# Optimization experiments

Hardware: AMD Instinct MI355X
Metric: run time of the kernel (lower is better)

The kernel has to match this reference:

```python
import jax, jax.numpy as jnp
import numpy as np

B, D, H, E, K = 4096, 1024, 4096, 8, 2

def setup_inputs() -> dict:
    key = jax.random.key(0)
    ks = jax.random.split(key, 6)
    return {
        "x_modality": jax.random.normal(ks[0], (B, D), dtype=jnp.float32),
        "expert_indices": jax.random.randint(ks[1], (B, K), 0, E, dtype=jnp.int32),
        "hard_weights": jax.random.uniform(ks[2], (B, K), dtype=jnp.float32),
        "w1": jax.random.normal(ks[3], (E, D, H), dtype=jnp.float32) * (1.0 / np.sqrt(D)),
        "b1": jnp.zeros((E, H), dtype=jnp.float32),
        "w2": jax.random.normal(ks[4], (E, H, D), dtype=jnp.float32) * (1.0 / np.sqrt(H)),
        "b2": jnp.zeros((E, D), dtype=jnp.float32),
    }

def reference(x_modality, expert_indices, hard_weights, w1, b1, w2, b2):
    b = x_modality.shape[0]
    # Per-token gate per expert: sum of hard_weights over top_k slots routed to that expert.
    gates = jnp.zeros((b, E), dtype=x_modality.dtype)
    gates = gates.at[jnp.arange(b)[:, None], expert_indices].add(hard_weights)  # [b, E]
    # Dense expert compute (small fixed E), then gated combine.
    h = jax.nn.gelu(jnp.einsum("bd,edh->ebh", x_modality, w1) + b1[:, None, :], approximate=False)
    y = jnp.einsum("ebh,ehd->ebd", h, w2) + b2[:, None, :]  # [E, b, D]
    return jnp.einsum("be,ebd->bd", gates, y)
```

## Files before the change

kernel.cpp:

```cpp
#include <hip/hip_runtime.h>
#include <hip/hip_bf16.h>
#include <math.h>

#define NB 4096
#define ND 1024
#define NH 4096
#define NE 8
#define NKK 2
#define NROWS (NB*NKK)
#define MAXT 72

typedef __attribute__((ext_vector_type(8))) short short8;
typedef __attribute__((ext_vector_type(4))) float f32x4;

__device__ __forceinline__ void gload_lds16(const void* g, void* l) {
    __builtin_amdgcn_global_load_lds(
        (const __attribute__((address_space(1))) unsigned int*)g,
        (__attribute__((address_space(3))) unsigned int*)l, 16, 0, 0);
}

__device__ __forceinline__ unsigned short f2bf(float f) {
    __hip_bfloat16 h = __float2bfloat16(f);
    return *reinterpret_cast<unsigned short*>(&h);
}

__device__ __forceinline__ float fast_gelu(float x) {
    float xs  = x * 0.70710678118654752f;
    float axs = fabsf(xs);
    float t   = __builtin_amdgcn_rcpf(1.0f + 0.3275911f * axs);
    float p   = t * (0.254829592f + t * (-0.284496736f + t * (1.421413741f +
                t * (-1.453152027f + t * 1.061405429f))));
    float e   = __expf(-xs * xs);
    float erf_abs = 1.0f - p * e;
    float erf = copysignf(erf_abs, x);
    return 0.5f * x * (1.0f + erf);
}


__global__ void k_cvt_x(const float* __restrict__ in, __hip_bfloat16* __restrict__ out, int n8) {
    int i = blockIdx.x * 256 + threadIdx.x;
    if (i >= n8) return;
    const float4* p = reinterpret_cast<const float4*>(in) + (size_t)i * 2;
    float4 a = p[0], b = p[1];
    ushort4 lo, hi;
    lo.x = f2bf(a.x); lo.y = f2bf(a.y); lo.z = f2bf(a.z); lo.w = f2bf(a.w);
    hi.x = f2bf(b.x); hi.y = f2bf(b.y); hi.z = f2bf(b.z); hi.w = f2bf(b.w);
    reinterpret_cast<ushort4*>(out)[(size_t)i*2]   = lo;
    reinterpret_cast<ushort4*>(out)[(size_t)i*2+1] = hi;
}

__global__ void k_transpose_cvt(const float* __restrict__ in, __hip_bfloat16* __restrict__ out,
                                int R, int C) {
    __shared__ float tile[64][68];
    const size_t ebase = (size_t)blockIdx.z * R * C;
    const int r0 = blockIdx.y * 64, c0 = blockIdx.x * 64;
    const int t = threadIdx.x;
    const int lr = t >> 4, lc4 = (t & 15) * 4;
    #pragma unroll
    for (int i = 0; i < 4; ++i) {
        int r = lr + i * 16;
        float4 v = *reinterpret_cast<const float4*>(&in[ebase + (size_t)(r0 + r) * C + (c0 + lc4)]);
        *reinterpret_cast<float4*>(&tile[r][lc4]) = v;
    }
    __syncthreads();
    const int q = t & 15, cw = t >> 4;
    #pragma unroll
    for (int i = 0; i < 4; ++i) {
        int cc = cw + i * 16;
        ushort4 v;
        v.x = f2bf(tile[q*4+0][cc]);
        v.y = f2bf(tile[q*4+1][cc]);
        v.z = f2bf(tile[q*4+2][cc]);
        v.w = f2bf(tile[q*4+3][cc]);
        *reinterpret_cast<ushort4*>(&out[ebase + (size_t)(c0 + cc) * R + (r0 + q*4)]) = v;
    }
}


__global__ void k_route_count(const int* __restrict__ idx, int* cnt) {
    int b = blockIdx.x * 256 + threadIdx.x;
    if (b < NB) {
        atomicAdd(&cnt[idx[2*b]], 1);
        atomicAdd(&cnt[idx[2*b+1]], 1);
    }
}

__global__ void k_route_scan(const int* __restrict__ cnt, int* offs, int* cursor,
                             int* tile_e, int* tile_row, int* ntiles) {
    if (threadIdx.x == 0) {
        int s = 0, t = 0;
        for (int e = 0; e < NE; ++e) {
            offs[e] = s; cursor[e] = s;
            for (int r = 0; r < cnt[e]; r += 128) {
                tile_e[t] = e; tile_row[t] = s + r; ++t;
            }
            s += cnt[e];
        }
        offs[NE] = s;
        *ntiles = t;
    }
}

__global__ void k_route_fill(const int* __restrict__ idx, const float* __restrict__ hw,
                             int* cursor, int* tok, float* gw) {
    int b = blockIdx.x * 256 + threadIdx.x;
    if (b < NB) {
        #pragma unroll
        for (int k = 0; k < NKK; ++k) {
            int e = idx[2*b + k];
            int p = atomicAdd(&cursor[e], 1);
            tok[p] = b;
            gw[p]  = hw[2*b + k];
        }
    }
}


template<int STAGE>
__global__ __launch_bounds__(256, 4) void moe_gemm(
    const __hip_bfloat16* __restrict__ Asrc,
    const __hip_bfloat16* __restrict__ Bt,
    const float* __restrict__ bias,
    __hip_bfloat16* __restrict__ Hout,
    float* __restrict__ Out,
    const int* __restrict__ offs,
    const int* __restrict__ tok,
    const float* __restrict__ gw,
    const int* __restrict__ tile_e,
    const int* __restrict__ tile_row,
    const int* __restrict__ ntiles)
{
    constexpr int N    = (STAGE == 1) ? NH : ND;
    constexpr int KROW = (STAGE == 1) ? ND : NH;
    constexpr int KT   = (STAGE == 1) ? 16 : 32;
    constexpr int TOTAL = (STAGE == 1) ? ((NH/128) * MAXT) : ((ND/128) * MAXT * 2);
    constexpr int CPX  = TOTAL / 8;

    const int bid = blockIdx.x;
    const int wgid = (bid & 7) * CPX + (bid >> 3);
    const int tile = wgid % MAXT;
    const int rest = wgid / MAXT;
    if (tile >= *ntiles) return;

    int nt, kbase;
    if (STAGE == 1) { nt = rest;     kbase = 0; }
    else            { nt = rest & 7; kbase = (rest >> 3) * (NH / 2); }

    const int e = tile_e[tile];
    const int rowbase = tile_row[tile];
    const int end = offs[e + 1];

    __shared__ __align__(16) __hip_bfloat16 sA[128 * 64];
    __shared__ __align__(16) __hip_bfloat16 sB[128 * 64];

    const int tid = threadIdx.x;
    const int w = tid >> 6;
    const int l = tid & 63;

    const int srow = tid >> 3;
    const int schunk = (tid & 7) ^ (srow & 7);
    const __hip_bfloat16* aptr[4];
    const __hip_bfloat16* bptr[4];
    #pragma unroll
    for (int i = 0; i < 4; ++i) {
        int r = srow + i * 32;
        int re = rowbase + r; if (re > end - 1) re = end - 1;
        if (STAGE == 1) aptr[i] = Asrc + (size_t)tok[re] * ND + schunk * 8;
        else            aptr[i] = Asrc + (size_t)re * NH + kbase + schunk * 8;
        bptr[i] = Bt + ((size_t)e * N + (nt * 128 + r)) * KROW + kbase + schunk * 8;
    }
    __hip_bfloat16 *adst[4], *bdst[4];
    #pragma unroll
    for (int i = 0; i < 4; ++i) {
        adst[i] = sA + (i * 256 + w * 64) * 8;
        bdst[i] = sB + (i * 256 + w * 64) * 8;
    }

    const int wm = (w >> 1) * 64;
    const int wn = (w & 1) * 64;
    const int l15 = l & 15, l4 = l >> 4;

    f32x4 acc[4][4];
    #pragma unroll
    for (int mi = 0; mi < 4; ++mi)
        #pragma unroll
        for (int ni = 0; ni < 4; ++ni) acc[mi][ni] = (f32x4){0.f, 0.f, 0.f, 0.f};

    int aoff[4][2], boff[4][2];
    #pragma unroll
    for (int mi = 0; mi < 4; ++mi) {
        int row = wm + mi * 16 + l15;
        #pragma unroll
        for (int ks = 0; ks < 2; ++ks)
            aoff[mi][ks] = row * 128 + (((ks * 4 + l4) ^ (row & 7)) * 16);
    }
    #pragma unroll
    for (int ni = 0; ni < 4; ++ni) {
        int row = wn + ni * 16 + l15;
        #pragma unroll
        for (int ks = 0; ks < 2; ++ks)
            boff[ni][ks] = row * 128 + (((ks * 4 + l4) ^ (row & 7)) * 16);
    }

    const char* sAb = (const char*)sA;
    const char* sBb = (const char*)sB;

    for (int kt = 0; kt < KT; ++kt) {
        #pragma unroll
        for (int i = 0; i < 4; ++i) {
            gload_lds16(aptr[i] + kt * 64, adst[i]);
            gload_lds16(bptr[i] + kt * 64, bdst[i]);
        }
        __syncthreads();
        short8 af[4][2], bfr[4][2];
        #pragma unroll
        for (int mi = 0; mi < 4; ++mi)
            #pragma unroll
            for (int ks = 0; ks < 2; ++ks)
                af[mi][ks] = *(const short8*)(sAb + aoff[mi][ks]);
        #pragma unroll
        for (int ni = 0; ni < 4; ++ni)
            #pragma unroll
            for (int ks = 0; ks < 2; ++ks)
                bfr[ni][ks] = *(const short8*)(sBb + boff[ni][ks]);
        #pragma unroll
        for (int mi = 0; mi < 4; ++mi)
            #pragma unroll
            for (int ni = 0; ni < 4; ++ni)
                #pragma unroll
                for (int ks = 0; ks < 2; ++ks)
                    acc[mi][ni] = __builtin_amdgcn_mfma_f32_16x16x32_bf16(
                        af[mi][ks], bfr[ni][ks], acc[mi][ni], 0, 0, 0);
        __syncthreads();
    }

    const int ncol0 = nt * 128 + wn;
    #pragma unroll
    for (int mi = 0; mi < 4; ++mi) {
        #pragma unroll
        for (int ni = 0; ni < 4; ++ni) {
            int gn = ncol0 + ni * 16 + l15;
            float bv = bias[e * N + gn];
            #pragma unroll
            for (int j = 0; j < 4; ++j) {
                int re = rowbase + wm + mi * 16 + l4 * 4 + j;
                if (re < end) {
                    float v = acc[mi][ni][j];
                    if (STAGE == 1) {
                        v += bv;
                        Hout[(size_t)re * NH + gn] = __float2bfloat16(fast_gelu(v));
                    } else {
                        if (kbase == 0) v += bv;
                        atomicAdd(&Out[(size_t)tok[re] * ND + gn], gw[re] * v);
                    }
                }
            }
        }
    }
}


extern "C" void kernel_launch(void* const* d_in, const int* in_sizes, int n_in,
                              void* d_out, int out_size, void* d_ws, size_t ws_size,
                              hipStream_t stream) {
    const float* x   = (const float*)d_in[0];
    const int*   idx = (const int*)d_in[1];
    const float* hw  = (const float*)d_in[2];
    const float* w1  = (const float*)d_in[3];
    const float* b1  = (const float*)d_in[4];
    const float* w2  = (const float*)d_in[5];
    const float* b2  = (const float*)d_in[6];
    float* out = (float*)d_out;

    char* ws = (char*)d_ws;
    size_t off = 0;
    __hip_bfloat16* xb  = (__hip_bfloat16*)(ws + off); off += (size_t)NB * ND * 2;
    __hip_bfloat16* w1t = (__hip_bfloat16*)(ws + off); off += (size_t)NE * ND * NH * 2;
    __hip_bfloat16* w2t = (__hip_bfloat16*)(ws + off); off += (size_t)NE * NH * ND * 2;
    __hip_bfloat16* h   = (__hip_bfloat16*)(ws + off); off += (size_t)NROWS * NH * 2;
    int*   tok     = (int*)(ws + off);   off += NROWS * 4;
    float* gwb     = (float*)(ws + off); off += NROWS * 4;
    int*   cnt     = (int*)(ws + off);   off += 16 * 4;
    int*   offs    = (int*)(ws + off);   off += 16 * 4;
    int*   cursor  = (int*)(ws + off);   off += 16 * 4;
    int*   tile_e  = (int*)(ws + off);   off += MAXT * 4;
    int*   tile_row= (int*)(ws + off);   off += MAXT * 4;
    int*   ntiles  = (int*)(ws + off);   off += 16 * 4;
    (void)ws_size; (void)in_sizes; (void)n_in; (void)out_size;

    hipMemsetAsync(d_out, 0, (size_t)NB * ND * sizeof(float), stream);
    hipMemsetAsync(cnt, 0, 16 * 4, stream);

    k_route_count<<<dim3((NB + 255) / 256), 256, 0, stream>>>(idx, cnt);
    k_route_scan<<<1, 64, 0, stream>>>(cnt, offs, cursor, tile_e, tile_row, ntiles);
    k_route_fill<<<dim3((NB + 255) / 256), 256, 0, stream>>>(idx, hw, cursor, tok, gwb);
    k_cvt_x<<<dim3((NB * ND / 8 + 255) / 256), 256, 0, stream>>>(x, xb, NB * ND / 8);

    k_transpose_cvt<<<dim3(NH / 64, ND / 64, NE), 256, 0, stream>>>(w1, w1t, ND, NH);
    moe_gemm<1><<<dim3((NH / 128) * MAXT), 256, 0, stream>>>(
        xb, w1t, b1, h, nullptr, offs, tok, gwb, tile_e, tile_row, ntiles);

    k_transpose_cvt<<<dim3(ND / 64, NH / 64, NE), 256, 0, stream>>>(w2, w2t, NH, ND);
    moe_gemm<2><<<dim3((ND / 128) * MAXT * 2), 256, 0, stream>>>(
        h, w2t, b2, nullptr, out, offs, tok, gwb, tile_e, tile_row, ntiles);
}
```

Before: 429.7 us.

## Widen stage-1 GEMM tile to 256 columns and drop stage-2 split-K

Stage 1 now uses a 128x256 output tile per workgroup with 4x8 MFMA fragments per wave and launch bounds lowered to 2 waves per EU. This halves the grid and raises reuse of the gathered activation rows. Stage 2 no longer splits K into two halves, which halves the atomic adds into the output. The price is fewer, longer workgroups and lower occupancy, with more register pressure in stage 1. The inner loop is restructured per k-step to shorten fragment lifetimes, and the weight conversion kernels are moved ahead of routing.

```diff
diff --git a/kernel.cpp b/kernel.cpp
--- a/kernel.cpp
+++ b/kernel.cpp
@@ -117,7 +117,7 @@
 
 
 template<int STAGE>
-__global__ __launch_bounds__(256, 4) void moe_gemm(
+__global__ __launch_bounds__(256, (STAGE == 1) ? 2 : 4) void moe_gemm(
     const __hip_bfloat16* __restrict__ Asrc,
     const __hip_bfloat16* __restrict__ Bt,
     const float* __restrict__ bias,
@@ -132,26 +132,25 @@
 {
     constexpr int N    = (STAGE == 1) ? NH : ND;
     constexpr int KROW = (STAGE == 1) ? ND : NH;
-    constexpr int KT   = (STAGE == 1) ? 16 : 32;
-    constexpr int TOTAL = (STAGE == 1) ? ((NH/128) * MAXT) : ((ND/128) * MAXT * 2);
+    constexpr int KT   = (STAGE == 1) ? 16 : 64;
+    constexpr int BN   = (STAGE == 1) ? 256 : 128;
+    constexpr int NF   = BN / 32;
+    constexpr int BLr  = BN / 32;
+    constexpr int TOTAL = (N / BN) * MAXT;
     constexpr int CPX  = TOTAL / 8;
 
     const int bid = blockIdx.x;
     const int wgid = (bid & 7) * CPX + (bid >> 3);
     const int tile = wgid % MAXT;
-    const int rest = wgid / MAXT;
+    const int nt   = wgid / MAXT;
     if (tile >= *ntiles) return;
-
-    int nt, kbase;
-    if (STAGE == 1) { nt = rest;     kbase = 0; }
-    else            { nt = rest & 7; kbase = (rest >> 3) * (NH / 2); }
 
     const int e = tile_e[tile];
     const int rowbase = tile_row[tile];
     const int end = offs[e + 1];
 
     __shared__ __align__(16) __hip_bfloat16 sA[128 * 64];
-    __shared__ __align__(16) __hip_bfloat16 sB[128 * 64];
+    __shared__ __align__(16) __hip_bfloat16 sB[BN * 64];
 
     const int tid = threadIdx.x;
     const int w = tid >> 6;
@@ -160,33 +159,37 @@
     const int srow = tid >> 3;
     const int schunk = (tid & 7) ^ (srow & 7);
     const __hip_bfloat16* aptr[4];
-    const __hip_bfloat16* bptr[4];
     #pragma unroll
     for (int i = 0; i < 4; ++i) {
         int r = srow + i * 32;
         int re = rowbase + r; if (re > end - 1) re = end - 1;
         if (STAGE == 1) aptr[i] = Asrc + (size_t)tok[re] * ND + schunk * 8;
-        else            aptr[i] = Asrc + (size_t)re * NH + kbase + schunk * 8;
-        bptr[i] = Bt + ((size_t)e * N + (nt * 128 + r)) * KROW + kbase + schunk * 8;
-    }
-    __hip_bfloat16 *adst[4], *bdst[4];
-    #pragma unroll
-    for (int i = 0; i < 4; ++i) {
+        else            aptr[i] = Asrc + (size_t)re * NH + schunk * 8;
+    }
+    const __hip_bfloat16* bptr[BLr];
+    #pragma unroll
+    for (int i = 0; i < BLr; ++i)
+        bptr[i] = Bt + ((size_t)e * N + (nt * BN + srow + i * 32)) * KROW + schunk * 8;
+
+    __hip_bfloat16 *adst[4], *bdst[BLr];
+    #pragma unroll
+    for (int i = 0; i < 4; ++i)
         adst[i] = sA + (i * 256 + w * 64) * 8;
+    #pragma unroll
+    for (int i = 0; i < BLr; ++i)
         bdst[i] = sB + (i * 256 + w * 64) * 8;
-    }
 
     const int wm = (w >> 1) * 64;
-    const int wn = (w & 1) * 64;
+    const int wn = (w & 1) * (BN / 2);
     const int l15 = l & 15, l4 = l >> 4;
 
-    f32x4 acc[4][4];
+    f32x4 acc[4][NF];
     #pragma unroll
     for (int mi = 0; mi < 4; ++mi)
         #pragma unroll
-        for (int ni = 0; ni < 4; ++ni) acc[mi][ni] = (f32x4){0.f, 0.f, 0.f, 0.f};
-
-    int aoff[4][2], boff[4][2];
+        for (int ni = 0; ni < NF; ++ni) acc[mi][ni] = (f32x4){0.f, 0.f, 0.f, 0.f};
+
+    int aoff[4][2], boff[NF][2];
     #pragma unroll
     for (int mi = 0; mi < 4; ++mi) {
         int row = wm + mi * 16 + l15;
@@ -195,7 +198,7 @@
             aoff[mi][ks] = row * 128 + (((ks * 4 + l4) ^ (row & 7)) * 16);
     }
     #pragma unroll
-    for (int ni = 0; ni < 4; ++ni) {
+    for (int ni = 0; ni < NF; ++ni) {
         int row = wn + ni * 16 + l15;
         #pragma unroll
         for (int ks = 0; ks < 2; ++ks)
@@ -205,52 +208,53 @@
     const char* sAb = (const char*)sA;
     const char* sBb = (const char*)sB;
 
+    #pragma unroll 1
     for (int kt = 0; kt < KT; ++kt) {
         #pragma unroll
-        for (int i = 0; i < 4; ++i) {
+        for (int i = 0; i < 4; ++i)
             gload_lds16(aptr[i] + kt * 64, adst[i]);
+        #pragma unroll
+        for (int i = 0; i < BLr; ++i)
             gload_lds16(bptr[i] + kt * 64, bdst[i]);
+        __syncthreads();
+        #pragma unroll
+        for (int ks = 0; ks < 2; ++ks) {
+            short8 af[4];
+            #pragma unroll
+            for (int mi = 0; mi < 4; ++mi)
+                af[mi] = *(const short8*)(sAb + aoff[mi][ks]);
+            #pragma unroll
+            for (int nh = 0; nh < NF / 4; ++nh) {
+                short8 bfr[4];
+                #pragma unroll
+                for (int nj = 0; nj < 4; ++nj)
+                    bfr[nj] = *(const short8*)(sBb + boff[nh * 4 + nj][ks]);
+                #pragma unroll
+                for (int mi = 0; mi < 4; ++mi)
+                    #pragma unroll
+                    for (int nj = 0; nj < 4; ++nj)
+                        acc[mi][nh * 4 + nj] = __builtin_amdgcn_mfma_f32_16x16x32_bf16(
+                            af[mi], bfr[nj], acc[mi][nh * 4 + nj], 0, 0, 0);
+            }
         }
         __syncthreads();
-        short8 af[4][2], bfr[4][2];
-        #pragma unroll
-        for (int mi = 0; mi < 4; ++mi)
-            #pragma unroll
-            for (int ks = 0; ks < 2; ++ks)
-                af[mi][ks] = *(const short8*)(sAb + aoff[mi][ks]);
-        #pragma unroll
-        for (int ni = 0; ni < 4; ++ni)
-            #pragma unroll
-            for (int ks = 0; ks < 2; ++ks)
-                bfr[ni][ks] = *(const short8*)(sBb + boff[ni][ks]);
-        #pragma unroll
-        for (int mi = 0; mi < 4; ++mi)
-            #pragma unroll
-            for (int ni = 0; ni < 4; ++ni)
-                #pragma unroll
-                for (int ks = 0; ks < 2; ++ks)
-                    acc[mi][ni] = __builtin_amdgcn_mfma_f32_16x16x32_bf16(
-                        af[mi][ks], bfr[ni][ks], acc[mi][ni], 0, 0, 0);
-        __syncthreads();
-    }
-
-    const int ncol0 = nt * 128 + wn;
+    }
+
+    const int ncol0 = nt * BN + wn;
     #pragma unroll
     for (int mi = 0; mi < 4; ++mi) {
         #pragma unroll
-        for (int ni = 0; ni < 4; ++ni) {
+        for (int ni = 0; ni < NF; ++ni) {
             int gn = ncol0 + ni * 16 + l15;
             float bv = bias[e * N + gn];
             #pragma unroll
             for (int j = 0; j < 4; ++j) {
                 int re = rowbase + wm + mi * 16 + l4 * 4 + j;
                 if (re < end) {
-                    float v = acc[mi][ni][j];
+                    float v = acc[mi][ni][j] + bv;
                     if (STAGE == 1) {
-                        v += bv;
                         Hout[(size_t)re * NH + gn] = __float2bfloat16(fast_gelu(v));
                     } else {
-                        if (kbase == 0) v += bv;
                         atomicAdd(&Out[(size_t)tok[re] * ND + gn], gw[re] * v);
                     }
                 }
@@ -291,16 +295,15 @@
     hipMemsetAsync(d_out, 0, (size_t)NB * ND * sizeof(float), stream);
     hipMemsetAsync(cnt, 0, 16 * 4, stream);
 
+    k_cvt_x<<<dim3((NB * ND / 8 + 255) / 256), 256, 0, stream>>>(x, xb, NB * ND / 8);
+    k_transpose_cvt<<<dim3(NH / 64, ND / 64, NE), 256, 0, stream>>>(w1, w1t, ND, NH);
+    k_transpose_cvt<<<dim3(ND / 64, NH / 64, NE), 256, 0, stream>>>(w2, w2t, NH, ND);
     k_route_count<<<dim3((NB + 255) / 256), 256, 0, stream>>>(idx, cnt);
     k_route_scan<<<1, 64, 0, stream>>>(cnt, offs, cursor, tile_e, tile_row, ntiles);
     k_route_fill<<<dim3((NB + 255) / 256), 256, 0, stream>>>(idx, hw, cursor, tok, gwb);
-    k_cvt_x<<<dim3((NB * ND / 8 + 255) / 256), 256, 0, stream>>>(x, xb, NB * ND / 8);
-
-    k_transpose_cvt<<<dim3(NH / 64, ND / 64, NE), 256, 0, stream>>>(w1, w1t, ND, NH);
-    moe_gemm<1><<<dim3((NH / 128) * MAXT), 256, 0, stream>>>(
+
+    moe_gemm<1><<<dim3((NH / 256) * MAXT), 256, 0, stream>>>(
         xb, w1t, b1, h, nullptr, offs, tok, gwb, tile_e, tile_row, ntiles);
-
-    k_transpose_cvt<<<dim3(ND / 64, NH / 64, NE), 256, 0, stream>>>(w2, w2t, NH, ND);
-    moe_gemm<2><<<dim3((ND / 128) * MAXT * 2), 256, 0, stream>>>(
+    moe_gemm<2><<<dim3((ND / 128) * MAXT), 256, 0, stream>>>(
         h, w2t, b2, nullptr, out, offs, tok, gwb, tile_e, tile_row, ntiles);
 }
```

After: 428.0 us. Within noise of the previous version (-0.4%).
